# Optimization experiments

Measured on AMD Instinct MI355X. Metric: run time of the kernel, lower is better.

## Reference

```python
import jax, jax.numpy as jnp
import numpy as np

B, T, K = 256, 512, 128


def _reverse_sequence(x, lens, axis_len):
    # Reverse the first lens[b] entries of x[b] along time axis (axis=1); rest unchanged.
    pos = jnp.arange(axis_len)[None, :]              # [1, T]
    idx = jnp.where(pos < lens[:, None], lens[:, None] - 1 - pos, pos)  # [B, T]
    if x.ndim == 3:
        idx = idx[:, :, None]
        idx = jnp.broadcast_to(idx, x.shape)
    return jnp.take_along_axis(x, idx, axis=1)


def setup_inputs() -> dict:
    key = jax.random.key(0)
    k1, k2, k3 = jax.random.split(key, 3)
    potentials = jax.random.normal(k1, (B, T, K), dtype=jnp.float32)
    sequence_lengths = jax.random.randint(k2, (B,), 1, T + 1, dtype=jnp.int32)
    # glorot_uniform for [K, K] transitions
    limit = np.sqrt(6.0 / (K + K))
    transitions = jax.random.uniform(k3, (K, K), dtype=jnp.float32,
                                     minval=-limit, maxval=limit)
    return {"potentials": potentials, "transitions": transitions,
            "sequence_lengths": sequence_lengths}


def _crf_decode(potentials, transitions, sequence_lengths):
    lens = sequence_lengths.astype(jnp.int32)
    num_tags = potentials.shape[-1]
    init_state = potentials[:, 0, :]                 # [B, K]
    inputs = potentials[:, 1:, :]                    # [B, T-1, K]
    lens_m1 = jnp.maximum(0, lens - 1)
    mask = jnp.arange(inputs.shape[1])[None, :] < lens_m1[:, None]  # [B, T-1]

    def fwd_step(state, xm):
        x, m = xm                                    # x [B,K], m [B]
        ts = state[:, :, None] + transitions[None]   # [B, K(prev), K(cur)]
        new_state = x + jnp.max(ts, axis=1)          # [B, K]
        bp = jnp.argmax(ts, axis=1).astype(jnp.int32)
        new_state = jnp.where(m[:, None], new_state, state)
        bp = jnp.where(m[:, None], bp, 0)
        return new_state, bp

    xs = (jnp.swapaxes(inputs, 0, 1), jnp.swapaxes(mask, 0, 1))
    last_score, bps = jax.lax.scan(fwd_step, init_state, xs)
    backpointers = jnp.swapaxes(bps, 0, 1)           # [B, T-1, K]
    backpointers = _reverse_sequence(backpointers, lens_m1, backpointers.shape[1])

    init_tag = jnp.argmax(last_score, axis=1).astype(jnp.int32)  # [B]

    def bwd_step(tag, bp):                           # tag [B], bp [B,K]
        new = jnp.take_along_axis(bp, tag[:, None], axis=1)[:, 0]
        return new, new

    _, tags = jax.lax.scan(bwd_step, init_tag, jnp.swapaxes(backpointers, 0, 1))
    decode_tags = jnp.concatenate([init_tag[:, None], jnp.swapaxes(tags, 0, 1)], axis=1)  # [B,T]
    decode_tags = _reverse_sequence(decode_tags, lens, decode_tags.shape[1])
    best_score = jnp.max(last_score, axis=1)
    return decode_tags, best_score


def reference(potentials, transitions, sequence_lengths):
    decode_tags, _ = _crf_decode(potentials, transitions, sequence_lengths)
    # inference-phase output: one-hot of Viterbi tags
    return jax.nn.one_hot(decode_tags, potentials.shape[-1], dtype=potentials.dtype)
```

## Files before the change

### kernel.cpp

```cpp
#include <hip/hip_runtime.h>

#define B_ 256
#define T_ 512
#define K_ 128
#define NT 256
#define DELTA 0.03125f

template<int CTRL>
__device__ __forceinline__ float dpp_fmax(float v) {
  int iv = __float_as_int(v);
  int t = __builtin_amdgcn_update_dpp(iv, iv, CTRL, 0xF, 0xF, false);
  return fmaxf(v, __int_as_float(t));
}
__device__ __forceinline__ float rlanef(float v, int lane) {
  return __int_as_float(__builtin_amdgcn_readlane(__float_as_int(v), lane));
}

__global__ __launch_bounds__(NT) void viterbi_fused(
    const float* __restrict__ pot,
    const float* __restrict__ trans,
    const int*   __restrict__ lens,
    float* __restrict__ out)
{
  extern __shared__ __align__(16) char smem[];
  float2*         Tp   = (float2*)smem;
  unsigned char*  bp   = (unsigned char*)(smem + 65536);
  unsigned short* code = (unsigned short*)(smem + 130944);
  unsigned char*  tags = (unsigned char*)(smem + 131968);
  int*            scr  = (int*)(smem + 132480);

  const int tid = threadIdx.x;
  const int b   = blockIdx.x;
  const int L   = lens[b];
  const float* potb = pot + (size_t)b * T_ * K_;

  float mn = INFINITY, mx = -INFINITY;
  for (int e = tid; e < K_ * 64; e += NT) {
    const int i = e >> 6, l = e & 63;
    const float a = trans[i * K_ + l];
    const float c = trans[i * K_ + l + 64];
    Tp[e] = make_float2(a, c);
    mn = fminf(mn, fminf(a, c));
    mx = fmaxf(mx, fmaxf(a, c));
  }
  float* red = (float*)bp;
  red[tid] = mn; red[NT + tid] = mx;
  __syncthreads();

  if (tid < 64) {
    const int l = tid;
    float rmn = INFINITY, rmx = -INFINITY;
#pragma unroll
    for (int i = 0; i < 4; ++i) {
      rmn = fminf(rmn, red[i * 64 + l]);
      rmx = fmaxf(rmx, red[256 + i * 64 + l]);
    }
    for (int d = 1; d < 64; d <<= 1) {
      rmn = fminf(rmn, __shfl_xor(rmn, d));
      rmx = fmaxf(rmx, __shfl_xor(rmx, d));
    }
    const float Rng = (rmx - rmn) + DELTA;

    float s0 = potb[l], s1 = potb[64 + l];
    float xa0 = potb[K_ + l], xa1 = potb[K_ + 64 + l];

    for (int t = 1; t < L; ++t) {
      const int tn = (t + 1 < L) ? t + 1 : t;
      const float xb0 = potb[tn * K_ + l];
      const float xb1 = potb[tn * K_ + 64 + l];

      float lm = fmaxf(s0, s1);
      lm = dpp_fmax<0x121>(lm);
      lm = dpp_fmax<0x122>(lm);
      lm = dpp_fmax<0x124>(lm);
      lm = dpp_fmax<0x128>(lm);
      lm = dpp_fmax<0x142>(lm);
      lm = dpp_fmax<0x143>(lm);
      const float M = rlanef(lm, 63);
      const float thr = M - Rng;

      unsigned long long c0m = __ballot(s0 >= thr);
      unsigned long long c1m = __ballot(s1 >= thr);
      int nc = __popcll(c0m) + __popcll(c1m);
      if (nc == 0) { c0m = ~0ull; c1m = ~0ull; nc = 128; }

      int c0; float sc;
      if (c0m) { c0 = __ffsll(c0m) - 1; c0m &= c0m - 1; sc = rlanef(s0, c0); }
      else     { int cc = __ffsll(c1m) - 1; c1m &= c1m - 1; sc = rlanef(s1, cc); c0 = cc + 64; }
      const float2 tv = Tp[(c0 << 6) + l];

      if (nc == 1) {
        s0 = xa0 + (sc + tv.x);
        s1 = xa1 + (sc + tv.y);
        if (l == 0) code[t - 1] = (unsigned short)c0;
      } else {
        float m0 = sc + tv.x, m1 = sc + tv.y;
        int i0 = c0, i1 = c0;
        int rem = nc - 1;
        while (rem--) {
          int c; float sv;
          if (c0m) { c = __ffsll(c0m) - 1; c0m &= c0m - 1; sv = rlanef(s0, c); }
          else     { int cc = __ffsll(c1m) - 1; c1m &= c1m - 1; sv = rlanef(s1, cc); c = cc + 64; }
          const float2 tc = Tp[(c << 6) + l];
          const float v0 = sv + tc.x, v1 = sv + tc.y;
          if (v0 > m0) { m0 = v0; i0 = c; }
          if (v1 > m1) { m1 = v1; i1 = c; }
        }
        s0 = xa0 + m0;
        s1 = xa1 + m1;
        bp[(t - 1) * K_ + l]      = (unsigned char)i0;
        bp[(t - 1) * K_ + 64 + l] = (unsigned char)i1;
        if (l == 0) code[t - 1] = 0xFFFF;
      }
      xa0 = xb0; xa1 = xb1;
    }

    float bv = s0; int bi = l;
    if (s1 > bv) { bv = s1; bi = l + 64; }
    for (int d = 1; d < 64; d <<= 1) {
      const float ov = __shfl_xor(bv, d);
      const int   oi = __shfl_xor(bi, d);
      if (ov > bv || (ov == bv && oi < bi)) { bv = ov; bi = oi; }
    }
    if (l == 0) { tags[L - 1] = (unsigned char)bi; scr[0] = bi; }
  }
  __syncthreads();

  const int bestTag = scr[0];
  for (int p = L + tid; p < T_; p += NT) tags[p] = 0;
  for (int p = tid; p < L - 1; p += NT) {
    const unsigned short c = code[p];
    if (c != 0xFFFF) {
      int tg = c;
      tags[p] = (unsigned char)tg;
      int q = p - 1;
      while (q >= 0 && code[q] == 0xFFFF) {
        tg = bp[q * K_ + tg];
        tags[q] = (unsigned char)tg;
        --q;
      }
    }
  }
  if (tid == 0 && L >= 2) {
    int tg = bestTag;
    int q = L - 2;
    while (q >= 0 && code[q] == 0xFFFF) {
      tg = bp[q * K_ + tg];
      tags[q] = (unsigned char)tg;
      --q;
    }
  }
  __syncthreads();

  float4* o4 = (float4*)(out + (size_t)b * T_ * K_);
  for (int i = tid; i < T_ * K_ / 4; i += NT) {
    const int p  = i >> 5;
    const int tg = tags[p];
    const int k  = (i & 31) * 4;
    float4 v;
    v.x = (k     == tg) ? 1.0f : 0.0f;
    v.y = (k + 1 == tg) ? 1.0f : 0.0f;
    v.z = (k + 2 == tg) ? 1.0f : 0.0f;
    v.w = (k + 3 == tg) ? 1.0f : 0.0f;
    o4[i] = v;
  }
}

extern "C" void kernel_launch(void* const* d_in, const int* in_sizes, int n_in,
                              void* d_out, int out_size, void* d_ws, size_t ws_size,
                              hipStream_t stream) {
  const float* pot   = (const float*)d_in[0];
  const float* trans = (const float*)d_in[1];
  const int*   lens  = (const int*)d_in[2];
  float* out = (float*)d_out;

  viterbi_fused<<<B_, NT, 132608, stream>>>(pot, trans, lens, out);
}
```

Before: 328.3 us.

## Unroll Viterbi forward loop by 8 with deep potential prefetch and batched candidate loads

Unrolls the serial forward recursion eight steps at a time and keeps eight time steps of emission potentials in registers, prefetched eight steps ahead, so global load latency is hidden behind several recursion steps. In the multi-candidate case it also issues the first up to four candidate readlanes and LDS transition loads before comparing them, exposing memory-level parallelism. This raises register pressure and code size substantially and adds an epilogue for leftover steps.

After: 311.0 us. -5.3%, faster.

```diff
diff --git a/kernel.cpp b/kernel.cpp
--- a/kernel.cpp
+++ b/kernel.cpp
@@ -14,6 +14,10 @@
 }
 __device__ __forceinline__ float rlanef(float v, int lane) {
   return __int_as_float(__builtin_amdgcn_readlane(__float_as_int(v), lane));
+}
+__device__ __forceinline__ int popcand(unsigned long long& m0, unsigned long long& m1) {
+  if (m0) { int c = __ffsll(m0) - 1; m0 &= m0 - 1; return c; }
+  int c = __ffsll(m1) - 1; m1 &= m1 - 1; return c + 64;
 }
 
 __global__ __launch_bounds__(NT) void viterbi_fused(
@@ -36,9 +40,9 @@
 
   float mn = INFINITY, mx = -INFINITY;
   for (int e = tid; e < K_ * 64; e += NT) {
-    const int i = e >> 6, l = e & 63;
-    const float a = trans[i * K_ + l];
-    const float c = trans[i * K_ + l + 64];
+    const int i = e >> 6, ll = e & 63;
+    const float a = trans[i * K_ + ll];
+    const float c = trans[i * K_ + ll + 64];
     Tp[e] = make_float2(a, c);
     mn = fminf(mn, fminf(a, c));
     mx = fmaxf(mx, fmaxf(a, c));
@@ -62,58 +66,93 @@
     const float Rng = (rmx - rmn) + DELTA;
 
     float s0 = potb[l], s1 = potb[64 + l];
-    float xa0 = potb[K_ + l], xa1 = potb[K_ + 64 + l];
-
-    for (int t = 1; t < L; ++t) {
-      const int tn = (t + 1 < L) ? t + 1 : t;
-      const float xb0 = potb[tn * K_ + l];
-      const float xb1 = potb[tn * K_ + 64 + l];
-
-      float lm = fmaxf(s0, s1);
-      lm = dpp_fmax<0x121>(lm);
-      lm = dpp_fmax<0x122>(lm);
-      lm = dpp_fmax<0x124>(lm);
-      lm = dpp_fmax<0x128>(lm);
-      lm = dpp_fmax<0x142>(lm);
-      lm = dpp_fmax<0x143>(lm);
-      const float M = rlanef(lm, 63);
-      const float thr = M - Rng;
-
-      unsigned long long c0m = __ballot(s0 >= thr);
-      unsigned long long c1m = __ballot(s1 >= thr);
-      int nc = __popcll(c0m) + __popcll(c1m);
-      if (nc == 0) { c0m = ~0ull; c1m = ~0ull; nc = 128; }
-
-      int c0; float sc;
-      if (c0m) { c0 = __ffsll(c0m) - 1; c0m &= c0m - 1; sc = rlanef(s0, c0); }
-      else     { int cc = __ffsll(c1m) - 1; c1m &= c1m - 1; sc = rlanef(s1, cc); c0 = cc + 64; }
-      const float2 tv = Tp[(c0 << 6) + l];
-
-      if (nc == 1) {
-        s0 = xa0 + (sc + tv.x);
-        s1 = xa1 + (sc + tv.y);
-        if (l == 0) code[t - 1] = (unsigned short)c0;
-      } else {
-        float m0 = sc + tv.x, m1 = sc + tv.y;
-        int i0 = c0, i1 = c0;
-        int rem = nc - 1;
-        while (rem--) {
-          int c; float sv;
-          if (c0m) { c = __ffsll(c0m) - 1; c0m &= c0m - 1; sv = rlanef(s0, c); }
-          else     { int cc = __ffsll(c1m) - 1; c1m &= c1m - 1; sv = rlanef(s1, cc); c = cc + 64; }
-          const float2 tc = Tp[(c << 6) + l];
-          const float v0 = sv + tc.x, v1 = sv + tc.y;
-          if (v0 > m0) { m0 = v0; i0 = c; }
-          if (v1 > m1) { m1 = v1; i1 = c; }
-        }
-        s0 = xa0 + m0;
-        s1 = xa1 + m1;
-        bp[(t - 1) * K_ + l]      = (unsigned char)i0;
-        bp[(t - 1) * K_ + 64 + l] = (unsigned char)i1;
-        if (l == 0) code[t - 1] = 0xFFFF;
-      }
-      xa0 = xb0; xa1 = xb1;
-    }
+
+    float e0_0, e1_0, e0_1, e1_1, e0_2, e1_2, e0_3, e1_3;
+    float e0_4, e1_4, e0_5, e1_5, e0_6, e1_6, e0_7, e1_7;
+#define PLOAD(KK)                                                     \
+    { int idx = 1 + KK; idx = (idx < L) ? idx : (L - 1);              \
+      const float* pp = potb + idx * K_;                              \
+      e0_##KK = pp[l]; e1_##KK = pp[64 + l]; }
+    PLOAD(0) PLOAD(1) PLOAD(2) PLOAD(3) PLOAD(4) PLOAD(5) PLOAD(6) PLOAD(7)
+
+#define VSTEP(KK, PREF)                                                        \
+    {                                                                          \
+      float lm = fmaxf(s0, s1);                                                \
+      lm = dpp_fmax<0x121>(lm);                                                \
+      lm = dpp_fmax<0x122>(lm);                                                \
+      lm = dpp_fmax<0x124>(lm);                                                \
+      lm = dpp_fmax<0x128>(lm);                                                \
+      lm = dpp_fmax<0x142>(lm);                                                \
+      lm = dpp_fmax<0x143>(lm);                                                \
+      const float M = rlanef(lm, 63);                                          \
+      const float thr = M - Rng;                                               \
+      unsigned long long c0m = __ballot(s0 >= thr);                            \
+      unsigned long long c1m = __ballot(s1 >= thr);                            \
+      int nc = __popcll(c0m) + __popcll(c1m);                                  \
+      if (nc == 0) { c0m = ~0ull; c1m = ~0ull; nc = 128; }                     \
+      const int ca = popcand(c0m, c1m);                                        \
+      const float sa = (ca < 64) ? rlanef(s0, ca) : rlanef(s1, ca - 64);       \
+      const float2 ta = Tp[(ca << 6) + l];                                     \
+      if (nc == 1) {                                                           \
+        const float a0 = sa + ta.x, a1 = sa + ta.y;                            \
+        s0 = e0_##KK + a0; s1 = e1_##KK + a1;                                  \
+        if (l == 0) code[t + KK - 1] = (unsigned short)ca;                     \
+      } else {                                                                 \
+        const int cb = popcand(c0m, c1m);                                      \
+        const float sb = (cb < 64) ? rlanef(s0, cb) : rlanef(s1, cb - 64);     \
+        const float2 tb = Tp[(cb << 6) + l];                                   \
+        int cc = ca, cd = ca; float scv = sa, sdv = sa;                        \
+        float2 tc = ta, td = ta;                                               \
+        if (nc >= 3) { cc = popcand(c0m, c1m);                                 \
+          scv = (cc < 64) ? rlanef(s0, cc) : rlanef(s1, cc - 64);              \
+          tc = Tp[(cc << 6) + l]; }                                            \
+        if (nc >= 4) { cd = popcand(c0m, c1m);                                 \
+          sdv = (cd < 64) ? rlanef(s0, cd) : rlanef(s1, cd - 64);              \
+          td = Tp[(cd << 6) + l]; }                                            \
+        float m0 = sa + ta.x, m1 = sa + ta.y; int i0 = ca, i1 = ca;            \
+        { const float v0 = sb + tb.x, v1 = sb + tb.y;                          \
+          if (v0 > m0) { m0 = v0; i0 = cb; }                                   \
+          if (v1 > m1) { m1 = v1; i1 = cb; } }                                 \
+        if (nc >= 3) { const float v0 = scv + tc.x, v1 = scv + tc.y;           \
+          if (v0 > m0) { m0 = v0; i0 = cc; }                                   \
+          if (v1 > m1) { m1 = v1; i1 = cc; } }                                 \
+        if (nc >= 4) { const float v0 = sdv + td.x, v1 = sdv + td.y;           \
+          if (v0 > m0) { m0 = v0; i0 = cd; }                                   \
+          if (v1 > m1) { m1 = v1; i1 = cd; } }                                 \
+        int rem = nc - 4;                                                      \
+        while (rem-- > 0) {                                                    \
+          const int c = popcand(c0m, c1m);                                     \
+          const float sv = (c < 64) ? rlanef(s0, c) : rlanef(s1, c - 64);      \
+          const float2 tv = Tp[(c << 6) + l];                                  \
+          const float v0 = sv + tv.x, v1 = sv + tv.y;                          \
+          if (v0 > m0) { m0 = v0; i0 = c; }                                    \
+          if (v1 > m1) { m1 = v1; i1 = c; }                                    \
+        }                                                                      \
+        s0 = e0_##KK + m0; s1 = e1_##KK + m1;                                  \
+        bp[(t + KK - 1) * K_ + l]      = (unsigned char)i0;                    \
+        bp[(t + KK - 1) * K_ + 64 + l] = (unsigned char)i1;                    \
+        if (l == 0) code[t + KK - 1] = 0xFFFF;                                 \
+      }                                                                        \
+      if (PREF) {                                                              \
+        int idx = t + KK + 8; idx = (idx < L) ? idx : (L - 1);                 \
+        const float* pp = potb + idx * K_;                                     \
+        e0_##KK = pp[l]; e1_##KK = pp[64 + l];                                 \
+      }                                                                        \
+    }
+
+    int t = 1;
+    while (t + 8 <= L) {
+      VSTEP(0, true) VSTEP(1, true) VSTEP(2, true) VSTEP(3, true)
+      VSTEP(4, true) VSTEP(5, true) VSTEP(6, true) VSTEP(7, true)
+      t += 8;
+    }
+    if (t + 0 < L) VSTEP(0, false)
+    if (t + 1 < L) VSTEP(1, false)
+    if (t + 2 < L) VSTEP(2, false)
+    if (t + 3 < L) VSTEP(3, false)
+    if (t + 4 < L) VSTEP(4, false)
+    if (t + 5 < L) VSTEP(5, false)
+    if (t + 6 < L) VSTEP(6, false)
 
     float bv = s0; int bi = l;
     if (s1 > bv) { bv = s1; bi = l + 64; }
```
